# Kernel tuning notes

Measured on AMD Instinct MI355X. Metric: run time of the kernel, lower is better.

## Reference

```python
import jax, jax.numpy as jnp
import numpy as np

B, N, C, H = 8, 4096, 768, 8
EPS = 1e-12  # F.normalize eps


def setup_inputs() -> dict:
    key = jax.random.key(0)
    k1, k2, k3, k4 = jax.random.split(key, 4)
    x = jax.random.normal(k1, (B, N, C), dtype=jnp.float32)
    Wqkv = jax.random.normal(k2, (C, 3 * C), dtype=jnp.float32) * (1.0 / np.sqrt(C))
    temperature = jnp.ones((H, 1, 1), dtype=jnp.float32)
    Wproj = jax.random.normal(k3, (C, C), dtype=jnp.float32) * (1.0 / np.sqrt(C))
    bproj = jax.random.normal(k4, (C,), dtype=jnp.float32) * 0.01
    return {"x": x, "Wqkv": Wqkv, "temperature": temperature, "Wproj": Wproj, "bproj": bproj}


def _l2norm(t):
    # F.normalize(dim=-1): t / max(||t||_2, eps)
    n = jnp.sqrt(jnp.sum(t * t, axis=-1, keepdims=True))
    return t / jnp.maximum(n, EPS)


def reference(x, Wqkv, temperature, Wproj, bproj):
    b, n, c = x.shape
    h = temperature.shape[0]
    hd = c // h
    qkv = x @ Wqkv  # [B, N, 3C]
    qkv = qkv.reshape(b, n, 3, h, hd).transpose(2, 0, 3, 4, 1)  # [3, B, H, hd, N]
    q, k, v = qkv[0], qkv[1], qkv[2]
    q = _l2norm(q)  # normalize over token dim N
    k = _l2norm(k)
    # channel-channel attention: [B, H, hd, hd]
    attn = jnp.einsum('bhdn,bhen->bhde', q, k) * temperature  # temperature [H,1,1] broadcasts
    attn = jax.nn.softmax(attn, axis=-1)
    out = jnp.einsum('bhde,bhen->bhdn', attn, v)  # [B, H, hd, N]
    out = out.transpose(0, 3, 1, 2).reshape(b, n, c)  # [B, N, C]
    return out @ Wproj + bproj
```

## Files before the change

kernel.cpp:

```cpp
#include <hip/hip_runtime.h>
#include <stdint.h>


typedef __attribute__((ext_vector_type(8))) __bf16 bf16x8;
typedef __attribute__((ext_vector_type(4))) float f32x4;

__device__ __forceinline__ unsigned short f2b(float f) {
  uint32_t u = __float_as_uint(f);
  u += 0x7FFF + ((u >> 16) & 1);
  return (unsigned short)(u >> 16);
}

__device__ __forceinline__ void gload16(const void* g, void* l) {
  __builtin_amdgcn_global_load_lds(
      (__attribute__((address_space(1))) void*)(uintptr_t)g,
      (__attribute__((address_space(3))) void*)(uintptr_t)l, 16, 0, 0);
}

__global__ void cvt_bf16(const float* __restrict__ in, unsigned short* __restrict__ out, int n4,
                         float* __restrict__ Z, int nz4) {
  int gid = blockIdx.x * blockDim.x + threadIdx.x;
  if (gid < nz4) reinterpret_cast<float4*>(Z)[gid] = make_float4(0.f, 0.f, 0.f, 0.f);
  int stride = gridDim.x * blockDim.x;
  for (int i = gid; i < n4; i += stride) {
    float4 v = reinterpret_cast<const float4*>(in)[i];
    ushort4 o;
    o.x = f2b(v.x); o.y = f2b(v.y); o.z = f2b(v.z); o.w = f2b(v.w);
    reinterpret_cast<ushort4*>(out)[i] = o;
  }
}

__global__ void cvt_transpose(const float* __restrict__ in, unsigned short* __restrict__ out,
                              int K, int NC) {
  __shared__ float tile[32][33];
  int bx = blockIdx.x, by = blockIdx.y;
  int tx = threadIdx.x & 31, ty = threadIdx.x >> 5;
  for (int r = ty; r < 32; r += 8)
    tile[r][tx] = in[(size_t)(by * 32 + r) * NC + bx * 32 + tx];
  __syncthreads();
  for (int r = ty; r < 32; r += 8)
    out[(size_t)(bx * 32 + r) * K + by * 32 + tx] = f2b(tile[tx][r]);
}

__global__ __launch_bounds__(256, 2) void gemm_qkv(
    const unsigned short* __restrict__ A, const unsigned short* __restrict__ Bt,
    unsigned short* __restrict__ qkT, unsigned short* __restrict__ vT,
    float* __restrict__ normsq) {
  __shared__ __align__(16) unsigned short lds[17408];
  int bj = blockIdx.x;
  int bm = blockIdx.y;
  int m0 = bm * 128, j0 = bj * 128;
  int tid = threadIdx.x;
  int wid = tid >> 6, lane = tid & 63;
  int wm = wid >> 1, wn = wid & 1;
  int quad = lane >> 4, l16 = lane & 15;
  int srow = lane >> 3, sch = lane & 7;
  int cmem = sch ^ srow;

  f32x4 acc[4][4];
  f32x4 z = {0.f, 0.f, 0.f, 0.f};
#pragma unroll
  for (int i = 0; i < 4; i++)
#pragma unroll
    for (int j = 0; j < 4; j++) acc[i][j] = z;

  const unsigned short* Ab = A + (size_t)m0 * 768;
  const unsigned short* Bb = Bt + (size_t)j0 * 768;

  for (int k0 = 0; k0 < 768; k0 += 64) {
#pragma unroll
    for (int i = 0; i < 4; i++) {
      int ig = wid * 4 + i;
      int row = ig * 8 + srow;
      gload16(Ab + (size_t)row * 768 + k0 + cmem * 8, &lds[ig * 512]);
      gload16(Bb + (size_t)row * 768 + k0 + cmem * 8, &lds[8192 + ig * 512]);
    }
    __syncthreads();
#pragma unroll
    for (int kk = 0; kk < 2; kk++) {
      int cs = ((kk * 4 + quad) ^ (l16 & 7)) * 8;
      bf16x8 af[4], bfr[4];
#pragma unroll
      for (int mi = 0; mi < 4; mi++)
        af[mi] = *(const bf16x8*)&lds[(wm * 64 + mi * 16 + l16) * 64 + cs];
#pragma unroll
      for (int ni = 0; ni < 4; ni++)
        bfr[ni] = *(const bf16x8*)&lds[8192 + (wn * 64 + ni * 16 + l16) * 64 + cs];
#pragma unroll
      for (int mi = 0; mi < 4; mi++)
#pragma unroll
        for (int ni = 0; ni < 4; ni++)
          acc[mi][ni] = __builtin_amdgcn_mfma_f32_16x16x32_bf16(af[mi], bfr[ni], acc[mi][ni], 0, 0, 0);
    }
    __syncthreads();
  }

  int s = bj / 6;
  int b = bm >> 5;
  int n0 = m0 & 4095;
  bool isv = (s == 2);

  if (!isv) {
#pragma unroll
    for (int ni = 0; ni < 4; ni++) {
      float ss = 0.f;
#pragma unroll
      for (int mi = 0; mi < 4; mi++)
#pragma unroll
        for (int r = 0; r < 4; r++) ss += acc[mi][ni][r] * acc[mi][ni][r];
      ss += __shfl_down(ss, 32, 64);
      ss += __shfl_down(ss, 16, 64);
      if (lane < 16) {
        int cc = wn * 64 + ni * 16 + l16;
        int local = j0 + cc - s * 768;
        int hh = local / 96, d = local - hh * 96;
        atomicAdd(&normsq[s * 6144 + (b * 8 + hh) * 96 + d], ss);
      }
    }
  }

#pragma unroll
  for (int mi = 0; mi < 4; mi++)
#pragma unroll
    for (int ni = 0; ni < 4; ni++)
#pragma unroll
      for (int r = 0; r < 4; r++) {
        int m = wm * 64 + mi * 16 + quad * 4 + r;
        int cc = wn * 64 + ni * 16 + l16;
        unsigned short v = f2b(acc[mi][ni][r]);
        lds[isv ? (m * 136 + cc) : (cc * 136 + m)] = v;
      }
  __syncthreads();
  if (!isv) {
#pragma unroll
    for (int it = 0; it < 8; it++) {
      int id = tid + it * 256;
      int jr = id >> 4, mc = id & 15;
      int j = j0 + jr;
      int hh = (j - s * 768) / 96;
      int d = j - s * 768 - hh * 96;
      size_t off = ((size_t)(s * 64 + b * 8 + hh) * 96 + d) * 4096 + n0 + mc * 8;
      *(uint4*)&qkT[off] = *(const uint4*)&lds[jr * 136 + mc * 8];
    }
  } else {
#pragma unroll
    for (int it = 0; it < 8; it++) {
      int id = tid + it * 256;
      int mr = id >> 4, ch = id & 15;
      int cp = (j0 - 1536) + ch * 8;
      int hh = cp / 96, e = cp - hh * 96;
      size_t off = ((size_t)(b * 8 + hh) * 4096 + (n0 + mr)) * 96 + e;
      *(uint4*)&vT[off] = *(const uint4*)&lds[mr * 136 + ch * 8];
    }
  }
}

__global__ __launch_bounds__(256, 2) void attn_s(const unsigned short* __restrict__ qkT,
                                                 float* __restrict__ S) {
  __shared__ __align__(16) unsigned short lds[12288];
  int blk = blockIdx.x;
  int bh = blk >> 3, ks = blk & 7;
  const unsigned short* qb = qkT + (size_t)bh * 96 * 4096;
  const unsigned short* kb = qkT + (size_t)(64 + bh) * 96 * 4096;
  int tid = threadIdx.x, wid = tid >> 6, lane = tid & 63;
  int wm = wid >> 1, wn = wid & 1, quad = lane >> 4, l16 = lane & 15;
  int srow = lane >> 3, sch = lane & 7;
  int cmem = sch ^ srow;
  f32x4 acc[3][3];
  f32x4 z = {0.f, 0.f, 0.f, 0.f};
#pragma unroll
  for (int i = 0; i < 3; i++)
#pragma unroll
    for (int j = 0; j < 3; j++) acc[i][j] = z;

  for (int k0 = ks * 512; k0 < ks * 512 + 512; k0 += 64) {
#pragma unroll
    for (int i = 0; i < 3; i++) {
      int ig = wid * 3 + i;
      int row = ig * 8 + srow;
      gload16(qb + (size_t)row * 4096 + k0 + cmem * 8, &lds[ig * 512]);
      gload16(kb + (size_t)row * 4096 + k0 + cmem * 8, &lds[6144 + ig * 512]);
    }
    __syncthreads();
#pragma unroll
    for (int kk = 0; kk < 2; kk++) {
      int cs = ((kk * 4 + quad) ^ (l16 & 7)) * 8;
      bf16x8 af[3], bfr[3];
#pragma unroll
      for (int mi = 0; mi < 3; mi++)
        af[mi] = *(const bf16x8*)&lds[(wm * 48 + mi * 16 + l16) * 64 + cs];
#pragma unroll
      for (int ni = 0; ni < 3; ni++)
        bfr[ni] = *(const bf16x8*)&lds[6144 + (wn * 48 + ni * 16 + l16) * 64 + cs];
#pragma unroll
      for (int mi = 0; mi < 3; mi++)
#pragma unroll
        for (int ni = 0; ni < 3; ni++)
          acc[mi][ni] = __builtin_amdgcn_mfma_f32_16x16x32_bf16(af[mi], bfr[ni], acc[mi][ni], 0, 0, 0);
    }
    __syncthreads();
  }
  float* Sb = S + (size_t)bh * 9216;
#pragma unroll
  for (int mi = 0; mi < 3; mi++)
#pragma unroll
    for (int ni = 0; ni < 3; ni++)
#pragma unroll
      for (int r = 0; r < 4; r++)
        atomicAdd(&Sb[(wm * 48 + mi * 16 + quad * 4 + r) * 96 + wn * 48 + ni * 16 + l16],
                  acc[mi][ni][r]);
}

__global__ __launch_bounds__(256, 2) void attn_v(
    const float* __restrict__ S, const float* __restrict__ normsq,
    const float* __restrict__ temp, const unsigned short* __restrict__ vT,
    unsigned short* __restrict__ U) {
  __shared__ __align__(16) unsigned short lds[23488];
  float* ik = (float*)&lds[23296];
  int blk = blockIdx.x;
  int bh = blk >> 5, nc = blk & 31;
  int b = bh >> 3, h = bh & 7;
  int n0 = nc * 128;
  int tid = threadIdx.x, wid = tid >> 6, lane = tid & 63;
  int wm = wid >> 1, wn = wid & 1, quad = lane >> 4, l16 = lane & 15;

  const unsigned short* vb = vT + (size_t)bh * 4096 * 96 + (size_t)n0 * 96;
#pragma unroll
  for (int i = 0; i < 7; i++) {
    int ig = wid + i * 4;
    if (ig < 26) {
      int id = ig * 64 + lane;
      int row = id / 13;
      int ch = id - row * 13;
      if (ch > 11) ch = 11;
      gload16(vb + (size_t)row * 96 + ch * 8, &lds[9984 + ig * 512]);
    }
  }

  if (tid < 96)
    ik[tid] = 1.0f / fmaxf(sqrtf(normsq[6144 + bh * 96 + tid]), 1e-12f);
  __syncthreads();

  if (tid < 96) {
    int d = tid;
    const float* Srow = S + (size_t)bh * 9216 + d * 96;
    float iq = (1.0f / fmaxf(sqrtf(normsq[bh * 96 + d]), 1e-12f)) * temp[h];
    float mx = -1e30f;
    for (int e = 0; e < 96; e++) mx = fmaxf(mx, Srow[e] * iq * ik[e]);
    float sum = 0.f;
    for (int e = 0; e < 96; e++) sum += __expf(Srow[e] * iq * ik[e] - mx);
    float inv = 1.0f / sum;
    for (int e = 0; e < 96; e++)
      lds[d * 104 + e] = f2b(__expf(Srow[e] * iq * ik[e] - mx) * inv);
  }
  __syncthreads();

  f32x4 acc[3][4];
  f32x4 z = {0.f, 0.f, 0.f, 0.f};
#pragma unroll
  for (int i = 0; i < 3; i++)
#pragma unroll
    for (int j = 0; j < 4; j++) acc[i][j] = z;
#pragma unroll
  for (int et = 0; et < 3; et++) {
    bf16x8 af[3], bfr[4];
#pragma unroll
    for (int mi = 0; mi < 3; mi++)
      af[mi] = *(const bf16x8*)&lds[(wm * 48 + mi * 16 + l16) * 104 + (et * 4 + quad) * 8];
#pragma unroll
    for (int ni = 0; ni < 4; ni++)
      bfr[ni] = *(const bf16x8*)&lds[9984 + (wn * 64 + ni * 16 + l16) * 104 + (et * 4 + quad) * 8];
#pragma unroll
    for (int mi = 0; mi < 3; mi++)
#pragma unroll
      for (int ni = 0; ni < 4; ni++)
        acc[mi][ni] = __builtin_amdgcn_mfma_f32_16x16x32_bf16(af[mi], bfr[ni], acc[mi][ni], 0, 0, 0);
  }
  __syncthreads();

#pragma unroll
  for (int mi = 0; mi < 3; mi++)
#pragma unroll
    for (int ni = 0; ni < 4; ni++)
#pragma unroll
      for (int r = 0; r < 4; r++) {
        int d = wm * 48 + mi * 16 + quad * 4 + r;
        int n = wn * 64 + ni * 16 + l16;
        lds[n * 104 + d] = f2b(acc[mi][ni][r]);
      }
  __syncthreads();
#pragma unroll
  for (int it = 0; it < 6; it++) {
    int id = tid + it * 256;
    int nr = id / 12, ch = id - nr * 12;
    *(uint4*)&U[((size_t)(b * 4096 + n0 + nr)) * 768 + h * 96 + ch * 8] =
        *(const uint4*)&lds[nr * 104 + ch * 8];
  }
}

__global__ __launch_bounds__(256, 2) void gemm_out(
    const unsigned short* __restrict__ A, const unsigned short* __restrict__ Bt,
    const float* __restrict__ bias, float* __restrict__ out) {
  __shared__ __align__(16) unsigned short lds[16384];
  int bj = blockIdx.x;
  int bm = blockIdx.y;
  int m0 = bm * 128, j0 = bj * 128;
  int tid = threadIdx.x;
  int wid = tid >> 6, lane = tid & 63;
  int wm = wid >> 1, wn = wid & 1;
  int quad = lane >> 4, l16 = lane & 15;
  int srow = lane >> 3, sch = lane & 7;
  int cmem = sch ^ srow;

  f32x4 acc[4][4];
  f32x4 z = {0.f, 0.f, 0.f, 0.f};
#pragma unroll
  for (int i = 0; i < 4; i++)
#pragma unroll
    for (int j = 0; j < 4; j++) acc[i][j] = z;

  const unsigned short* Ab = A + (size_t)m0 * 768;
  const unsigned short* Bb = Bt + (size_t)j0 * 768;

  for (int k0 = 0; k0 < 768; k0 += 64) {
#pragma unroll
    for (int i = 0; i < 4; i++) {
      int ig = wid * 4 + i;
      int row = ig * 8 + srow;
      gload16(Ab + (size_t)row * 768 + k0 + cmem * 8, &lds[ig * 512]);
      gload16(Bb + (size_t)row * 768 + k0 + cmem * 8, &lds[8192 + ig * 512]);
    }
    __syncthreads();
#pragma unroll
    for (int kk = 0; kk < 2; kk++) {
      int cs = ((kk * 4 + quad) ^ (l16 & 7)) * 8;
      bf16x8 af[4], bfr[4];
#pragma unroll
      for (int mi = 0; mi < 4; mi++)
        af[mi] = *(const bf16x8*)&lds[(wm * 64 + mi * 16 + l16) * 64 + cs];
#pragma unroll
      for (int ni = 0; ni < 4; ni++)
        bfr[ni] = *(const bf16x8*)&lds[8192 + (wn * 64 + ni * 16 + l16) * 64 + cs];
#pragma unroll
      for (int mi = 0; mi < 4; mi++)
#pragma unroll
        for (int ni = 0; ni < 4; ni++)
          acc[mi][ni] = __builtin_amdgcn_mfma_f32_16x16x32_bf16(af[mi], bfr[ni], acc[mi][ni], 0, 0, 0);
    }
    __syncthreads();
  }
#pragma unroll
  for (int ni = 0; ni < 4; ni++) {
    int ccol = j0 + wn * 64 + ni * 16 + l16;
    float bv = bias[ccol];
#pragma unroll
    for (int mi = 0; mi < 4; mi++)
#pragma unroll
      for (int r = 0; r < 4; r++)
        out[(size_t)(m0 + wm * 64 + mi * 16 + quad * 4 + r) * 768 + ccol] = acc[mi][ni][r] + bv;
  }
}

extern "C" void kernel_launch(void* const* d_in, const int* in_sizes, int n_in,
                              void* d_out, int out_size, void* d_ws, size_t ws_size,
                              hipStream_t stream) {
  const float* x = (const float*)d_in[0];
  const float* Wqkv = (const float*)d_in[1];
  const float* temp = (const float*)d_in[2];
  const float* Wproj = (const float*)d_in[3];
  const float* bproj = (const float*)d_in[4];
  float* out = (float*)d_out;
  char* ws = (char*)d_ws;

  unsigned short* xb     = (unsigned short*)(ws);
  unsigned short* WqkvT  = (unsigned short*)(ws + 50331648);
  unsigned short* WprojT = (unsigned short*)(ws + 53870592);
  unsigned short* qkT    = (unsigned short*)(ws + 55050240);
  unsigned short* vT     = (unsigned short*)(ws + 155713536);
  unsigned short* U      = (unsigned short*)(ws + 206045184);
  float* S               = (float*)(ws + 256376832);
  float* normsq          = (float*)(ws + 258736128);

  cvt_bf16<<<dim3(4096), dim3(256), 0, stream>>>(x, xb, 25165824 / 4, S, 150528);
  cvt_transpose<<<dim3(72, 24), dim3(256), 0, stream>>>(Wqkv, WqkvT, 768, 2304);
  cvt_transpose<<<dim3(24, 24), dim3(256), 0, stream>>>(Wproj, WprojT, 768, 768);
  gemm_qkv<<<dim3(18, 256), dim3(256), 0, stream>>>(xb, WqkvT, qkT, vT, normsq);
  attn_s<<<dim3(512), dim3(256), 0, stream>>>(qkT, S);
  attn_v<<<dim3(2048), dim3(256), 0, stream>>>(S, normsq, temp, vT, U);
  gemm_out<<<dim3(6, 256), dim3(256), 0, stream>>>(U, WprojT, bproj, out);
}
```

Before: 479.1 us.

## Compute channel attention via per-batch Gram matrix instead of materializing Q and K

Q and K are no longer produced token by token. The kernel builds the per-batch Gram matrix G = XᵀX (symmetric, upper-triangle tiles mirrored by atomics), projects it through the QKV weights, and forms both the q·k scores and the q/k row norms from WqᵀGWk and the matching diagonals. This removes two thirds of the large QKV GEMM and the big qkT round trip through memory. Only the V projection stays at full token size. Softmax moves into its own small kernel that writes bf16 attention probabilities for attn_v. In exchange it adds a transposed bf16 copy of x, extra launches and fp32 atomics. Rounding G to bf16 before the projection may reduce accuracy, and computing norms through G carries cancellation risk.

Measured after the change: 582.0 us. +21.5%, slower.

```diff
diff --git a/kernel.cpp b/kernel.cpp
--- a/kernel.cpp
+++ b/kernel.cpp
@@ -10,6 +10,9 @@
   u += 0x7FFF + ((u >> 16) & 1);
   return (unsigned short)(u >> 16);
 }
+__device__ __forceinline__ float b2f(unsigned short h) {
+  return __uint_as_float(((uint32_t)h) << 16);
+}
 
 __device__ __forceinline__ void gload16(const void* g, void* l) {
   __builtin_amdgcn_global_load_lds(
@@ -17,12 +20,61 @@
       (__attribute__((address_space(3))) void*)(uintptr_t)l, 16, 0, 0);
 }
 
-__global__ void cvt_bf16(const float* __restrict__ in, unsigned short* __restrict__ out, int n4,
-                         float* __restrict__ Z, int nz4) {
-  int gid = blockIdx.x * blockDim.x + threadIdx.x;
-  if (gid < nz4) reinterpret_cast<float4*>(Z)[gid] = make_float4(0.f, 0.f, 0.f, 0.f);
+__device__ __forceinline__ float dot8(uint4 a, uint4 b) {
+  float s = 0.f;
+  const uint32_t* pa = (const uint32_t*)&a;
+  const uint32_t* pb = (const uint32_t*)&b;
+#pragma unroll
+  for (int i = 0; i < 4; i++) {
+    s += b2f((unsigned short)(pa[i] & 0xffff)) * b2f((unsigned short)(pb[i] & 0xffff));
+    s += b2f((unsigned short)(pa[i] >> 16)) * b2f((unsigned short)(pb[i] >> 16));
+  }
+  return s;
+}
+
+__global__ __launch_bounds__(256) void cvt_dual(const float* __restrict__ x,
+                                                unsigned short* __restrict__ xb,
+                                                unsigned short* __restrict__ xT,
+                                                float* __restrict__ G) {
+  int tid = threadIdx.x;
+  int gid = (blockIdx.y * 512 + blockIdx.x) * 256 + tid;
+  if (gid < 1179648) reinterpret_cast<float4*>(G)[gid] = make_float4(0.f, 0.f, 0.f, 0.f);
+  __shared__ float tile[64][65];
+  int n0 = blockIdx.x * 64, c0 = blockIdx.y * 64;
+#pragma unroll
+  for (int it = 0; it < 4; it++) {
+    int slot = tid + it * 256;
+    int row = slot >> 4, c16 = slot & 15;
+    float4 v = *(const float4*)&x[(size_t)(n0 + row) * 768 + c0 + c16 * 4];
+    tile[row][c16 * 4 + 0] = v.x; tile[row][c16 * 4 + 1] = v.y;
+    tile[row][c16 * 4 + 2] = v.z; tile[row][c16 * 4 + 3] = v.w;
+  }
+  __syncthreads();
+  int b = n0 >> 12, nl = n0 & 4095;
+#pragma unroll
+  for (int it = 0; it < 2; it++) {
+    int slot = tid + it * 256;
+    int row = slot >> 3, cg = slot & 7;
+    unsigned short tmp[8];
+#pragma unroll
+    for (int j = 0; j < 8; j++) tmp[j] = f2b(tile[row][cg * 8 + j]);
+    *(uint4*)&xb[(size_t)(n0 + row) * 768 + c0 + cg * 8] = *(const uint4*)tmp;
+  }
+#pragma unroll
+  for (int it = 0; it < 2; it++) {
+    int slot = tid + it * 256;
+    int crow = slot >> 3, ng = slot & 7;
+    unsigned short tmp[8];
+#pragma unroll
+    for (int j = 0; j < 8; j++) tmp[j] = f2b(tile[ng * 8 + j][crow]);
+    *(uint4*)&xT[(size_t)b * 3145728 + (size_t)(c0 + crow) * 4096 + nl + ng * 8] =
+        *(const uint4*)tmp;
+  }
+}
+
+__global__ void cvt_bf16(const float* __restrict__ in, unsigned short* __restrict__ out, int n4) {
   int stride = gridDim.x * blockDim.x;
-  for (int i = gid; i < n4; i += stride) {
+  for (int i = blockIdx.x * blockDim.x + threadIdx.x; i < n4; i += stride) {
     float4 v = reinterpret_cast<const float4*>(in)[i];
     ushort4 o;
     o.x = f2b(v.x); o.y = f2b(v.y); o.z = f2b(v.z); o.w = f2b(v.w);
@@ -42,10 +94,9 @@
     out[(size_t)(bx * 32 + r) * K + by * 32 + tx] = f2b(tile[tx][r]);
 }
 
-__global__ __launch_bounds__(256, 2) void gemm_qkv(
+__global__ __launch_bounds__(256, 2) void gemm_v(
     const unsigned short* __restrict__ A, const unsigned short* __restrict__ Bt,
-    unsigned short* __restrict__ qkT, unsigned short* __restrict__ vT,
-    float* __restrict__ normsq) {
+    unsigned short* __restrict__ vT) {
   __shared__ __align__(16) unsigned short lds[17408];
   int bj = blockIdx.x;
   int bm = blockIdx.y;
@@ -65,7 +116,7 @@
     for (int j = 0; j < 4; j++) acc[i][j] = z;
 
   const unsigned short* Ab = A + (size_t)m0 * 768;
-  const unsigned short* Bb = Bt + (size_t)j0 * 768;
+  const unsigned short* Bb = Bt + (size_t)(1536 + j0) * 768;
 
   for (int k0 = 0; k0 < 768; k0 += 64) {
 #pragma unroll
@@ -95,30 +146,8 @@
     __syncthreads();
   }
 
-  int s = bj / 6;
   int b = bm >> 5;
   int n0 = m0 & 4095;
-  bool isv = (s == 2);
-
-  if (!isv) {
-#pragma unroll
-    for (int ni = 0; ni < 4; ni++) {
-      float ss = 0.f;
-#pragma unroll
-      for (int mi = 0; mi < 4; mi++)
-#pragma unroll
-        for (int r = 0; r < 4; r++) ss += acc[mi][ni][r] * acc[mi][ni][r];
-      ss += __shfl_down(ss, 32, 64);
-      ss += __shfl_down(ss, 16, 64);
-      if (lane < 16) {
-        int cc = wn * 64 + ni * 16 + l16;
-        int local = j0 + cc - s * 768;
-        int hh = local / 96, d = local - hh * 96;
-        atomicAdd(&normsq[s * 6144 + (b * 8 + hh) * 96 + d], ss);
-      }
-    }
-  }
-
 #pragma unroll
   for (int mi = 0; mi < 4; mi++)
 #pragma unroll
@@ -127,45 +156,181 @@
       for (int r = 0; r < 4; r++) {
         int m = wm * 64 + mi * 16 + quad * 4 + r;
         int cc = wn * 64 + ni * 16 + l16;
-        unsigned short v = f2b(acc[mi][ni][r]);
-        lds[isv ? (m * 136 + cc) : (cc * 136 + m)] = v;
+        lds[m * 136 + cc] = f2b(acc[mi][ni][r]);
       }
   __syncthreads();
-  if (!isv) {
-#pragma unroll
-    for (int it = 0; it < 8; it++) {
-      int id = tid + it * 256;
-      int jr = id >> 4, mc = id & 15;
-      int j = j0 + jr;
-      int hh = (j - s * 768) / 96;
-      int d = j - s * 768 - hh * 96;
-      size_t off = ((size_t)(s * 64 + b * 8 + hh) * 96 + d) * 4096 + n0 + mc * 8;
-      *(uint4*)&qkT[off] = *(const uint4*)&lds[jr * 136 + mc * 8];
-    }
-  } else {
-#pragma unroll
-    for (int it = 0; it < 8; it++) {
-      int id = tid + it * 256;
-      int mr = id >> 4, ch = id & 15;
-      int cp = (j0 - 1536) + ch * 8;
-      int hh = cp / 96, e = cp - hh * 96;
-      size_t off = ((size_t)(b * 8 + hh) * 4096 + (n0 + mr)) * 96 + e;
-      *(uint4*)&vT[off] = *(const uint4*)&lds[mr * 136 + ch * 8];
-    }
-  }
-}
-
-__global__ __launch_bounds__(256, 2) void attn_s(const unsigned short* __restrict__ qkT,
-                                                 float* __restrict__ S) {
-  __shared__ __align__(16) unsigned short lds[12288];
-  int blk = blockIdx.x;
-  int bh = blk >> 3, ks = blk & 7;
-  const unsigned short* qb = qkT + (size_t)bh * 96 * 4096;
-  const unsigned short* kb = qkT + (size_t)(64 + bh) * 96 * 4096;
+#pragma unroll
+  for (int it = 0; it < 8; it++) {
+    int id = tid + it * 256;
+    int mr = id >> 4, ch = id & 15;
+    int cp = j0 + ch * 8;
+    int hh = cp / 96, e = cp - hh * 96;
+    size_t off = ((size_t)(b * 8 + hh) * 4096 + (n0 + mr)) * 96 + e;
+    *(uint4*)&vT[off] = *(const uint4*)&lds[mr * 136 + ch * 8];
+  }
+}
+
+__global__ __launch_bounds__(256, 2) void gemm_G(const unsigned short* __restrict__ xT,
+                                                 float* __restrict__ G) {
+  __shared__ __align__(16) unsigned short lds[16384];
+  int t = blockIdx.x;
+  int ti = 0;
+  while (t >= ti + 1) { t -= ti + 1; ti++; }
+  int tj = t;
+  int z = blockIdx.y;
+  int b = z >> 2, ks = z & 3;
+  int kbase = ks * 1024;
+  int tid = threadIdx.x;
+  int wid = tid >> 6, lane = tid & 63;
+  int wm = wid >> 1, wn = wid & 1;
+  int quad = lane >> 4, l16 = lane & 15;
+  int srow = lane >> 3, sch = lane & 7;
+  int cmem = sch ^ srow;
+
+  f32x4 acc[4][4];
+  f32x4 zz = {0.f, 0.f, 0.f, 0.f};
+#pragma unroll
+  for (int i = 0; i < 4; i++)
+#pragma unroll
+    for (int j = 0; j < 4; j++) acc[i][j] = zz;
+
+  const unsigned short* Ab = xT + (size_t)b * 3145728 + (size_t)(ti * 128) * 4096 + kbase;
+  const unsigned short* Bb = xT + (size_t)b * 3145728 + (size_t)(tj * 128) * 4096 + kbase;
+
+  for (int k0 = 0; k0 < 1024; k0 += 64) {
+#pragma unroll
+    for (int i = 0; i < 4; i++) {
+      int ig = wid * 4 + i;
+      int row = ig * 8 + srow;
+      gload16(Ab + (size_t)row * 4096 + k0 + cmem * 8, &lds[ig * 512]);
+      gload16(Bb + (size_t)row * 4096 + k0 + cmem * 8, &lds[8192 + ig * 512]);
+    }
+    __syncthreads();
+#pragma unroll
+    for (int kk = 0; kk < 2; kk++) {
+      int cs = ((kk * 4 + quad) ^ (l16 & 7)) * 8;
+      bf16x8 af[4], bfr[4];
+#pragma unroll
+      for (int mi = 0; mi < 4; mi++)
+        af[mi] = *(const bf16x8*)&lds[(wm * 64 + mi * 16 + l16) * 64 + cs];
+#pragma unroll
+      for (int ni = 0; ni < 4; ni++)
+        bfr[ni] = *(const bf16x8*)&lds[8192 + (wn * 64 + ni * 16 + l16) * 64 + cs];
+#pragma unroll
+      for (int mi = 0; mi < 4; mi++)
+#pragma unroll
+        for (int ni = 0; ni < 4; ni++)
+          acc[mi][ni] = __builtin_amdgcn_mfma_f32_16x16x32_bf16(af[mi], bfr[ni], acc[mi][ni], 0, 0, 0);
+    }
+    __syncthreads();
+  }
+
+  float* Gb = G + (size_t)b * 589824;
+  bool mirror = (ti != tj);
+#pragma unroll
+  for (int mi = 0; mi < 4; mi++)
+#pragma unroll
+    for (int ni = 0; ni < 4; ni++)
+#pragma unroll
+      for (int r = 0; r < 4; r++) {
+        int gi = ti * 128 + wm * 64 + mi * 16 + quad * 4 + r;
+        int gj = tj * 128 + wn * 64 + ni * 16 + l16;
+        float v = acc[mi][ni][r];
+        atomicAdd(&Gb[(size_t)gi * 768 + gj], v);
+        if (mirror) atomicAdd(&Gb[(size_t)gj * 768 + gi], v);
+      }
+}
+
+__global__ __launch_bounds__(256, 2) void gemm_P(
+    const unsigned short* __restrict__ Gbf, const unsigned short* __restrict__ Wt,
+    unsigned short* __restrict__ PT) {
+  __shared__ __align__(16) unsigned short lds[17408];
+  int bj = blockIdx.x;
+  int bi = blockIdx.y;
+  int b = blockIdx.z;
+  int j0 = bj * 128, ci0 = bi * 128;
+  int tid = threadIdx.x;
+  int wid = tid >> 6, lane = tid & 63;
+  int wm = wid >> 1, wn = wid & 1;
+  int quad = lane >> 4, l16 = lane & 15;
+  int srow = lane >> 3, sch = lane & 7;
+  int cmem = sch ^ srow;
+
+  f32x4 acc[4][4];
+  f32x4 z = {0.f, 0.f, 0.f, 0.f};
+#pragma unroll
+  for (int i = 0; i < 4; i++)
+#pragma unroll
+    for (int j = 0; j < 4; j++) acc[i][j] = z;
+
+  const unsigned short* Ab = Gbf + (size_t)b * 589824 + (size_t)ci0 * 768;
+  const unsigned short* Bb = Wt + (size_t)j0 * 768;
+
+  for (int k0 = 0; k0 < 768; k0 += 64) {
+#pragma unroll
+    for (int i = 0; i < 4; i++) {
+      int ig = wid * 4 + i;
+      int row = ig * 8 + srow;
+      gload16(Ab + (size_t)row * 768 + k0 + cmem * 8, &lds[ig * 512]);
+      gload16(Bb + (size_t)row * 768 + k0 + cmem * 8, &lds[8192 + ig * 512]);
+    }
+    __syncthreads();
+#pragma unroll
+    for (int kk = 0; kk < 2; kk++) {
+      int cs = ((kk * 4 + quad) ^ (l16 & 7)) * 8;
+      bf16x8 af[4], bfr[4];
+#pragma unroll
+      for (int mi = 0; mi < 4; mi++)
+        af[mi] = *(const bf16x8*)&lds[(wm * 64 + mi * 16 + l16) * 64 + cs];
+#pragma unroll
+      for (int ni = 0; ni < 4; ni++)
+        bfr[ni] = *(const bf16x8*)&lds[8192 + (wn * 64 + ni * 16 + l16) * 64 + cs];
+#pragma unroll
+      for (int mi = 0; mi < 4; mi++)
+#pragma unroll
+        for (int ni = 0; ni < 4; ni++)
+          acc[mi][ni] = __builtin_amdgcn_mfma_f32_16x16x32_bf16(af[mi], bfr[ni], acc[mi][ni], 0, 0, 0);
+    }
+    __syncthreads();
+  }
+
+#pragma unroll
+  for (int mi = 0; mi < 4; mi++)
+#pragma unroll
+    for (int ni = 0; ni < 4; ni++)
+#pragma unroll
+      for (int r = 0; r < 4; r++) {
+        int m = wm * 64 + mi * 16 + quad * 4 + r;
+        int cc = wn * 64 + ni * 16 + l16;
+        lds[cc * 136 + m] = f2b(acc[mi][ni][r]);
+      }
+  __syncthreads();
+#pragma unroll
+  for (int it = 0; it < 8; it++) {
+    int id = tid + it * 256;
+    int jr = id >> 4, mc = id & 15;
+    size_t off = ((size_t)(b * 1536 + j0 + jr)) * 768 + ci0 + mc * 8;
+    *(uint4*)&PT[off] = *(const uint4*)&lds[jr * 136 + mc * 8];
+  }
+}
+
+__global__ __launch_bounds__(256, 2) void attn_softmax(
+    const unsigned short* __restrict__ Wt, const unsigned short* __restrict__ PT,
+    const float* __restrict__ temp, unsigned short* __restrict__ attnP) {
+  __shared__ __align__(16) char smem[39168];
+  unsigned short* stg = (unsigned short*)smem;
+  float* Sf = (float*)smem;
+  float* ninv = (float*)(smem + 38400);
+  int bh = blockIdx.x;
+  int b = bh >> 3, h = bh & 7;
   int tid = threadIdx.x, wid = tid >> 6, lane = tid & 63;
   int wm = wid >> 1, wn = wid & 1, quad = lane >> 4, l16 = lane & 15;
   int srow = lane >> 3, sch = lane & 7;
   int cmem = sch ^ srow;
+
+  const unsigned short* Arow = Wt + (size_t)(h * 96) * 768;
+  const unsigned short* Brow = PT + (size_t)(b * 1536 + 768 + h * 96) * 768;
+
   f32x4 acc[3][3];
   f32x4 z = {0.f, 0.f, 0.f, 0.f};
 #pragma unroll
@@ -173,13 +338,13 @@
 #pragma unroll
     for (int j = 0; j < 3; j++) acc[i][j] = z;
 
-  for (int k0 = ks * 512; k0 < ks * 512 + 512; k0 += 64) {
+  for (int k0 = 0; k0 < 768; k0 += 64) {
 #pragma unroll
     for (int i = 0; i < 3; i++) {
       int ig = wid * 3 + i;
       int row = ig * 8 + srow;
-      gload16(qb + (size_t)row * 4096 + k0 + cmem * 8, &lds[ig * 512]);
-      gload16(kb + (size_t)row * 4096 + k0 + cmem * 8, &lds[6144 + ig * 512]);
+      gload16(Arow + (size_t)row * 768 + k0 + cmem * 8, &stg[ig * 512]);
+      gload16(Brow + (size_t)row * 768 + k0 + cmem * 8, &stg[6144 + ig * 512]);
     }
     __syncthreads();
 #pragma unroll
@@ -188,10 +353,10 @@
       bf16x8 af[3], bfr[3];
 #pragma unroll
       for (int mi = 0; mi < 3; mi++)
-        af[mi] = *(const bf16x8*)&lds[(wm * 48 + mi * 16 + l16) * 64 + cs];
+        af[mi] = *(const bf16x8*)&stg[(wm * 48 + mi * 16 + l16) * 64 + cs];
 #pragma unroll
       for (int ni = 0; ni < 3; ni++)
-        bfr[ni] = *(const bf16x8*)&lds[6144 + (wn * 48 + ni * 16 + l16) * 64 + cs];
+        bfr[ni] = *(const bf16x8*)&stg[6144 + (wn * 48 + ni * 16 + l16) * 64 + cs];
 #pragma unroll
       for (int mi = 0; mi < 3; mi++)
 #pragma unroll
@@ -200,23 +365,54 @@
     }
     __syncthreads();
   }
-  float* Sb = S + (size_t)bh * 9216;
+
 #pragma unroll
   for (int mi = 0; mi < 3; mi++)
 #pragma unroll
     for (int ni = 0; ni < 3; ni++)
 #pragma unroll
       for (int r = 0; r < 4; r++)
-        atomicAdd(&Sb[(wm * 48 + mi * 16 + quad * 4 + r) * 96 + wn * 48 + ni * 16 + l16],
-                  acc[mi][ni][r]);
+        Sf[(wm * 48 + mi * 16 + quad * 4 + r) * 100 + wn * 48 + ni * 16 + l16] = acc[mi][ni][r];
+
+  if (tid < 192) {
+    int qsel = tid < 96 ? 0 : 1;
+    int d = tid - qsel * 96;
+    const unsigned short* wrow = Wt + (size_t)(qsel * 768 + h * 96 + d) * 768;
+    const unsigned short* prow = PT + (size_t)(b * 1536 + qsel * 768 + h * 96 + d) * 768;
+    float s = 0.f;
+#pragma unroll 4
+    for (int c8 = 0; c8 < 96; c8++)
+      s += dot8(*(const uint4*)&wrow[c8 * 8], *(const uint4*)&prow[c8 * 8]);
+    ninv[tid] = 1.0f / fmaxf(sqrtf(fmaxf(s, 0.f)), 1e-12f);
+  }
+  __syncthreads();
+
+  if (tid < 96) {
+    int d = tid;
+    float iq = ninv[d] * temp[h];
+    float mx = -1e30f;
+    for (int e = 0; e < 96; e++) mx = fmaxf(mx, Sf[d * 100 + e] * iq * ninv[96 + e]);
+    float sum = 0.f;
+    for (int e = 0; e < 96; e++) sum += __expf(Sf[d * 100 + e] * iq * ninv[96 + e] - mx);
+    float inv = 1.0f / sum;
+    for (int e = 0; e < 96; e++)
+      Sf[d * 100 + e] = __expf(Sf[d * 100 + e] * iq * ninv[96 + e] - mx) * inv;
+  }
+  __syncthreads();
+
+  for (int idx = tid; idx < 1152; idx += 256) {
+    int row = idx / 12, ch = idx - row * 12;
+    unsigned short tmp[8];
+#pragma unroll
+    for (int j = 0; j < 8; j++) tmp[j] = f2b(Sf[row * 100 + ch * 8 + j]);
+    *(uint4*)&attnP[(size_t)bh * 9216 + row * 96 + ch * 8] = *(const uint4*)tmp;
+  }
 }
 
 __global__ __launch_bounds__(256, 2) void attn_v(
-    const float* __restrict__ S, const float* __restrict__ normsq,
-    const float* __restrict__ temp, const unsigned short* __restrict__ vT,
+    const unsigned short* __restrict__ attnP, const unsigned short* __restrict__ vT,
     unsigned short* __restrict__ U) {
-  __shared__ __align__(16) unsigned short lds[23488];
-  float* ik = (float*)&lds[23296];
+  __shared__ __align__(16) unsigned short lds[23296];
   int blk = blockIdx.x;
   int bh = blk >> 5, nc = blk & 31;
   int b = bh >> 3, h = bh & 7;
@@ -236,22 +432,9 @@
       gload16(vb + (size_t)row * 96 + ch * 8, &lds[9984 + ig * 512]);
     }
   }
-
-  if (tid < 96)
-    ik[tid] = 1.0f / fmaxf(sqrtf(normsq[6144 + bh * 96 + tid]), 1e-12f);
-  __syncthreads();
-
-  if (tid < 96) {
-    int d = tid;
-    const float* Srow = S + (size_t)bh * 9216 + d * 96;
-    float iq = (1.0f / fmaxf(sqrtf(normsq[bh * 96 + d]), 1e-12f)) * temp[h];
-    float mx = -1e30f;
-    for (int e = 0; e < 96; e++) mx = fmaxf(mx, Srow[e] * iq * ik[e]);
-    float sum = 0.f;
-    for (int e = 0; e < 96; e++) sum += __expf(Srow[e] * iq * ik[e] - mx);
-    float inv = 1.0f / sum;
-    for (int e = 0; e < 96; e++)
-      lds[d * 104 + e] = f2b(__expf(Srow[e] * iq * ik[e] - mx) * inv);
+  for (int idx = tid; idx < 1152; idx += 256) {
+    int row = idx / 12, ch = idx - row * 12;
+    *(uint4*)&lds[row * 104 + ch * 8] = *(const uint4*)&attnP[(size_t)bh * 9216 + row * 96 + ch * 8];
   }
   __syncthreads();
 
@@ -375,17 +558,22 @@
   unsigned short* xb     = (unsigned short*)(ws);
   unsigned short* WqkvT  = (unsigned short*)(ws + 50331648);
   unsigned short* WprojT = (unsigned short*)(ws + 53870592);
-  unsigned short* qkT    = (unsigned short*)(ws + 55050240);
-  unsigned short* vT     = (unsigned short*)(ws + 155713536);
-  unsigned short* U      = (unsigned short*)(ws + 206045184);
-  float* S               = (float*)(ws + 256376832);
-  float* normsq          = (float*)(ws + 258736128);
-
-  cvt_bf16<<<dim3(4096), dim3(256), 0, stream>>>(x, xb, 25165824 / 4, S, 150528);
+  unsigned short* xT     = (unsigned short*)(ws + 55050240);
+  unsigned short* vT     = (unsigned short*)(ws + 105381888);
+  unsigned short* U      = (unsigned short*)(ws + 155713536);
+  float* G               = (float*)(ws + 206045184);
+  unsigned short* Gbf    = (unsigned short*)(ws + 224919552);
+  unsigned short* PT     = (unsigned short*)(ws + 234356736);
+  unsigned short* attnP  = (unsigned short*)(ws + 253231104);
+
+  cvt_dual<<<dim3(512, 12), dim3(256), 0, stream>>>(x, xb, xT, G);
   cvt_transpose<<<dim3(72, 24), dim3(256), 0, stream>>>(Wqkv, WqkvT, 768, 2304);
   cvt_transpose<<<dim3(24, 24), dim3(256), 0, stream>>>(Wproj, WprojT, 768, 768);
-  gemm_qkv<<<dim3(18, 256), dim3(256), 0, stream>>>(xb, WqkvT, qkT, vT, normsq);
-  attn_s<<<dim3(512), dim3(256), 0, stream>>>(qkT, S);
-  attn_v<<<dim3(2048), dim3(256), 0, stream>>>(S, normsq, temp, vT, U);
+  gemm_v<<<dim3(6, 256), dim3(256), 0, stream>>>(xb, WqkvT, vT);
+  gemm_G<<<dim3(21, 32), dim3(256), 0, stream>>>(xT, G);
+  cvt_bf16<<<dim3(2048), dim3(256), 0, stream>>>(G, Gbf, 1179648);
+  gemm_P<<<dim3(12, 6, 8), dim3(256), 0, stream>>>(Gbf, WqkvT, PT);
+  attn_softmax<<<dim3(64), dim3(256), 0, stream>>>(WqkvT, PT, temp, attnP);
+  attn_v<<<dim3(2048), dim3(256), 0, stream>>>(attnP, vT, U);
   gemm_out<<<dim3(6, 256), dim3(256), 0, stream>>>(U, WprojT, bproj, out);
 }
```
